# Kernel optimization log

Measured on AMD Instinct MI355X. Metric: run time of the kernel, lower is better.

Reference implementation:

```python
import jax, jax.numpy as jnp
import numpy as np

# MANO prior contact vertex indices (f1+f2+f3+f4+f5+f0 from CMap_loss3)
_F1 = [697,698,699,700,712,713,714,715,737,738,739,740,741,743,744,745,746,748,749,750,753,754,755,756,757,758,759,760,761,762,763,764,765,766,767,768]
_F2 = [46,47,48,49,164,165,166,167,194,195,223,237,238,280,281,298,301,317,320,323,324,325,326,327,328,329,330,331,332,333,340,341,342,343,344,345,346,347,348,349,350,351,352,353,354,355]
_F3 = [356,357,358,359,375,376,386,387,396,397,402,403,413,429,433,434,435,436,437,438,439,440,441,442,443,444,452,453,454,455,456,459,460,461,462,463,464,465,466,467]
_F4 = [468,469,470,471,484,485,486,496,497,506,507,513,514,524,545,546,547,548,549,550,551,552,553,555,563,564,565,566,567,570,572,573,574,575,576,577,578]
_F5 = [580,581,582,583,600,601,602,614,615,624,625,630,631,641,663,664,665,666,667,668,670,672,680,681,682,683,684,686,687,688,689,690,691,692,693,694,695]
_F0 = [73,96,98,99,772,774,775,777]
PRIOR_IDX = np.array(_F1 + _F2 + _F3 + _F4 + _F5 + _F0, dtype=np.int32)


def _sqdist(a, b):
    # a: [B,N,3], b: [B,M,3] -> squared distances [B,N,M] via ||a||^2+||b||^2-2ab
    a2 = jnp.sum(a * a, -1)          # [B,N]
    b2 = jnp.sum(b * b, -1)          # [B,M]
    ab = jnp.einsum('bnd,bmd->bnm', a, b)
    return jnp.maximum(a2[:, :, None] + b2[:, None, :] - 2.0 * ab, 0.0)


def _knn1(src, trg):
    # nearest neighbor (K=1): squared dists + indices, like pytorch3d knn_points
    d2 = _sqdist(src, trg)           # [B,N,M]
    return jnp.min(d2, -1), jnp.argmin(d2, -1)


def _verts_normals(verts, faces):
    # area-weighted vertex normals (pytorch3d verts_normals_packed)
    v0 = verts[:, faces[:, 0]]       # [B,F,3]
    v1 = verts[:, faces[:, 1]]
    v2 = verts[:, faces[:, 2]]
    fn = jnp.cross(v1 - v0, v2 - v0)
    vn = jnp.zeros_like(verts)
    vn = vn.at[:, faces[:, 0]].add(fn).at[:, faces[:, 1]].add(fn).at[:, faces[:, 2]].add(fn)
    return vn / (jnp.linalg.norm(vn, axis=-1, keepdims=True) + 1e-12)


def setup_inputs() -> dict:
    key = jax.random.key(0)
    ks = jax.random.split(key, 8)
    B, N1, V, F, Z, P = 64, 8192, 778, 1538, 64, 61
    scale = 0.1  # keep points in a 0.1 box so contact thresholds (0.005/0.01) fire
    return {
        'obj_xyz': jax.random.uniform(ks[0], (B, N1, 3), jnp.float32) * scale,
        'recon_xyz': jax.random.uniform(ks[1], (B, V, 3), jnp.float32) * scale,
        'gt_xyz': jax.random.uniform(ks[2], (B, V, 3), jnp.float32) * scale,
        'mean': jax.random.normal(ks[3], (B, Z), jnp.float32),
        'log_var': jax.random.normal(ks[4], (B, Z), jnp.float32),
        'recon_param': jax.random.normal(ks[5], (B, P), jnp.float32),
        'x_param': jax.random.normal(ks[6], (B, P), jnp.float32),
        'faces': jax.random.randint(ks[7], (F, 3), 0, V, jnp.int32),
    }


def reference(obj_xyz, recon_xyz, gt_xyz, mean, log_var, recon_param, x_param, faces):
    B = obj_xyz.shape[0]
    fB = jnp.float32(B)

    # KNN from object points to gt / reconstructed hand (squared dists)
    d_gt, _ = _knn1(obj_xyz, gt_xyz)            # [B,N1]
    d_rec, idx_rec = _knn1(obj_xyz, recon_xyz)  # [B,N1], [B,N1]

    # param loss: MSE sum / B
    param_loss = jnp.sum((recon_param - x_param) ** 2) / fB

    # CVAE loss: chamfer (point_reduction='sum', batch_reduction='mean') + KLD
    d2 = _sqdist(recon_xyz, gt_xyz)             # [B,778,778]
    recon_loss = jnp.mean(jnp.sum(jnp.min(d2, -1), -1)) + jnp.mean(jnp.sum(jnp.min(d2, -2), -1))
    KLD = -0.5 * jnp.sum(1.0 + log_var - mean ** 2 - jnp.exp(log_var)) / fB * 10.0
    cvae_loss = recon_loss + KLD

    # CMap_loss3: obj NN distance to prior hand contact verts, masked by cmap
    cmap = d_rec < 0.01 ** 2                    # [B,N1] bool
    prior = recon_xyz[:, PRIOR_IDX, :]          # [B,222,3]
    obj_CD, _ = _knn1(obj_xyz, prior)           # [B,N1]
    n_points = jnp.sum(cmap).astype(jnp.float32)
    cmap_loss = 3000.0 * jnp.sum(jnp.where(cmap, obj_CD, 0.0)) / (fB * n_points)

    # CMap consistency: contact-map overlap ratio
    recon_cmap = jnp.sqrt(d_rec) < 0.005
    gt_cmap = jnp.sqrt(d_gt) < 0.005
    gt_cnum = jnp.sum(gt_cmap).astype(jnp.float32) + 0.0001
    consistency_loss = -5.0 * jnp.sum(recon_cmap & gt_cmap).astype(jnp.float32) / gt_cnum

    # inter-penetration: gather NN hand verts/normals, sign of dot, masked dist sum
    vn = _verts_normals(recon_xyz, faces)                               # [B,778,3]
    nn_v = jnp.take_along_axis(recon_xyz, idx_rec[..., None], axis=1)   # [B,N1,3]
    nn_n = jnp.take_along_axis(vn, idx_rec[..., None], axis=1)          # [B,N1,3]
    interior = jnp.sum((nn_v - obj_xyz) * nn_n, -1) > 0                 # [B,N1]
    penetr_loss = 100.0 * jnp.sum(jnp.where(interior, d_rec, 0.0)) / fB

    a, b, c, d, e = 1.0, 0.1, 1000.0, 10.0, 10.0
    loss = a * cvae_loss + b * param_loss + c * cmap_loss + d * consistency_loss + e * penetr_loss
    return loss
```

## Files before the change

kernel.cpp:

```cpp
#include <hip/hip_runtime.h>
#include <math.h>

#define NB     64
#define N1V    8192
#define NPTS   (NB * N1V)
#define NV     778
#define NVP    780
#define NQ     195
#define SEG1Q  51
#define NFACE  1538
#define NZ     64
#define NPAR   61
#define NPRIOR 204
#define PPT    8
#define BIAS   0.0625f

#define REC_BLOCKS 256
#define GT_BLOCKS  256
#define CH_BLOCKS  128
#define NROLE_BLOCKS (REC_BLOCKS + GT_BLOCKS + CH_BLOCKS)
#define CMB_BLOCKS 64

#define BATCH_F4 2352
#define ACC_OFF (NB * BATCH_F4 * 4)
#define RC_OFF  (ACC_OFF + 16)
#define GC_OFF  (RC_OFF + NPTS / 32)

__device__ __constant__ int c_prior[NPRIOR] = {
  697,698,699,700,712,713,714,715,737,738,739,740,741,743,744,745,746,748,749,750,
  753,754,755,756,757,758,759,760,761,762,763,764,765,766,767,768,
  46,47,48,49,164,165,166,167,194,195,223,237,238,280,281,298,301,317,320,323,
  324,325,326,327,328,329,330,331,332,333,340,341,342,343,344,345,346,347,348,349,
  350,351,352,353,354,355,
  356,357,358,359,375,376,386,387,396,397,402,403,413,429,433,434,435,436,437,438,
  439,440,441,442,443,444,452,453,454,455,456,459,460,461,462,463,464,465,466,467,
  468,469,470,471,484,485,486,496,497,506,507,513,514,524,545,546,547,548,549,550,
  551,552,553,555,563,564,565,566,567,570,572,573,574,575,576,577,578,
  580,581,582,583,600,601,602,614,615,624,625,630,631,641,663,664,665,666,667,668,
  670,672,680,681,682,683,684,686,687,688,689,690,691,692,693,694,695,
  73,96,98,99,772,774,775,777
};

__global__ __launch_bounds__(256) void k_prep(const float* __restrict__ recon,
                                              const float* __restrict__ gt,
                                              const int* __restrict__ faces,
                                              float4* __restrict__ ws4,
                                              float* __restrict__ acc) {
    int b = blockIdx.x, tid = threadIdx.x;
    if (b == 0 && tid < 16) acc[tid] = 0.0f;
    __shared__ float4 s_r[NV];
    __shared__ float s_vnx[NV], s_vny[NV], s_vnz[NV];
    __shared__ unsigned int s_bm[25];
    __shared__ unsigned short s_pre[26];
    __shared__ unsigned short s_perm[NV];

    if (tid < 25) s_bm[tid] = 0u;
    __syncthreads();
    if (tid < NPRIOR) {
        int v = c_prior[tid];
        atomicOr(&s_bm[v >> 5], 1u << (v & 31));
    }
    const float* rb = recon + (size_t)b * NV * 3;
    const float* gb = gt    + (size_t)b * NV * 3;
    float4* gt4   = ws4 + (size_t)b * BATCH_F4;
    float4* rec4p = gt4 + NVP;
    float4* nrm4p = rec4p + NVP;
    for (int j = tid; j < NV; j += 256) {
        float x = rb[3*j], y = rb[3*j+1], z = rb[3*j+2];
        s_r[j] = make_float4(x, y, z, x*x + y*y + z*z + BIAS);
        x = gb[3*j]; y = gb[3*j+1]; z = gb[3*j+2];
        gt4[j] = make_float4(x, y, z, x*x + y*y + z*z);
        s_vnx[j] = 0.0f; s_vny[j] = 0.0f; s_vnz[j] = 0.0f;
    }
    if (tid < 2) gt4[NV + tid] = make_float4(0.f, 0.f, 0.f, 1e30f);
    __syncthreads();
    if (tid == 0) {
        unsigned int run = 0;
        for (int w = 0; w < 25; ++w) { s_pre[w] = (unsigned short)run; run += __popc(s_bm[w]); }
        s_pre[25] = (unsigned short)run;
    }
    __syncthreads();
    for (int j = tid; j < NV; j += 256) {
        int w = j >> 5;
        unsigned int below = s_bm[w] & ((1u << (j & 31)) - 1u);
        int rank = s_pre[w] + __popc(below);
        bool member = (s_bm[w] >> (j & 31)) & 1u;
        int pos = member ? rank : (NPRIOR + (j - rank));
        s_perm[pos] = (unsigned short)j;
    }
    for (int f = tid; f < NFACE; f += 256) {
        int i0 = faces[3*f], i1 = faces[3*f+1], i2 = faces[3*f+2];
        float4 p0 = s_r[i0], p1 = s_r[i1], p2 = s_r[i2];
        float e1x = p1.x - p0.x, e1y = p1.y - p0.y, e1z = p1.z - p0.z;
        float e2x = p2.x - p0.x, e2y = p2.y - p0.y, e2z = p2.z - p0.z;
        float fx = e1y * e2z - e1z * e2y;
        float fy = e1z * e2x - e1x * e2z;
        float fz = e1x * e2y - e1y * e2x;
        atomicAdd(&s_vnx[i0], fx); atomicAdd(&s_vny[i0], fy); atomicAdd(&s_vnz[i0], fz);
        atomicAdd(&s_vnx[i1], fx); atomicAdd(&s_vny[i1], fy); atomicAdd(&s_vnz[i1], fz);
        atomicAdd(&s_vnx[i2], fx); atomicAdd(&s_vny[i2], fy); atomicAdd(&s_vnz[i2], fz);
    }
    __syncthreads();
    for (int j = tid; j < NVP; j += 256) {
        if (j < NV) {
            int src = s_perm[j];
            rec4p[j] = s_r[src];
            float x = s_vnx[src], y = s_vny[src], z = s_vnz[src];
            float inv = 1.0f / (sqrtf(x*x + y*y + z*z) + 1e-12f);
            nrm4p[j] = make_float4(x * inv, y * inv, z * inv, 0.0f);
        } else {
            rec4p[j] = make_float4(0.f, 0.f, 0.f, 1e30f);
            nrm4p[j] = make_float4(0.f, 0.f, 1.f, 0.0f);
        }
    }
}

#define LOAD_PTS(ob)                                                          \
    const float4* ob4 = (const float4*)((ob) + (size_t)tid * 24);             \
    float4 q0 = ob4[0], q1 = ob4[1], q2 = ob4[2],                             \
           q3 = ob4[3], q4 = ob4[4], q5 = ob4[5];                             \
    float px[PPT], py[PPT], pz[PPT];                                          \
    px[0]=q0.x; py[0]=q0.y; pz[0]=q0.z;  px[1]=q0.w; py[1]=q1.x; pz[1]=q1.y;  \
    px[2]=q1.z; py[2]=q1.w; pz[2]=q2.x;  px[3]=q2.y; py[3]=q2.z; pz[3]=q2.w;  \
    px[4]=q3.x; py[4]=q3.y; pz[4]=q3.z;  px[5]=q3.w; py[5]=q4.x; pz[5]=q4.y;  \
    px[6]=q4.z; py[6]=q4.w; pz[6]=q5.x;  px[7]=q5.y; py[7]=q5.z; pz[7]=q5.w;

__global__ __launch_bounds__(256) void k_fused(const float* __restrict__ obj,
                                               const float4* __restrict__ ws4,
                                               float* __restrict__ acc,
                                               unsigned char* __restrict__ rcA,
                                               unsigned char* __restrict__ gcA) {
    __shared__ float4 s_t[NVP];
    __shared__ float s_red[3];
    int tid = threadIdx.x;
    int blk = blockIdx.x;

    if (blk < REC_BLOCKS) {
        int b = blk >> 2, chunk = blk & 3;
        const float4* base = ws4 + (size_t)b * BATCH_F4;
        const float4* rec4p = base + NVP;
        const float4* nrm4p = base + 2 * NVP;
        for (int j = tid; j < NVP; j += 256) s_t[j] = rec4p[j];
        if (tid < 3) s_red[tid] = 0.0f;
        __syncthreads();

        const float* ob = obj + ((size_t)b * N1V + (size_t)chunk * 2048) * 3;
        LOAD_PTS(ob)
        float nax[PPT], nay[PPT], naz[PPT], m[PPT];
        int q[PPT];
#pragma unroll
        for (int i = 0; i < PPT; ++i) {
            nax[i] = -2.0f * px[i]; nay[i] = -2.0f * py[i]; naz[i] = -2.0f * pz[i];
            m[i] = 3.4e38f; q[i] = 0;
        }
        float mp[PPT];
#pragma unroll 1
        for (int jq = 0; jq < SEG1Q; ++jq) {
            int j = 4 * jq;
            float4 t0 = s_t[j], t1 = s_t[j+1], t2 = s_t[j+2], t3 = s_t[j+3];
#pragma unroll
            for (int i = 0; i < PPT; ++i) {
                float d0 = fmaf(nax[i], t0.x, fmaf(nay[i], t0.y, fmaf(naz[i], t0.z, t0.w)));
                float d1 = fmaf(nax[i], t1.x, fmaf(nay[i], t1.y, fmaf(naz[i], t1.z, t1.w)));
                float d2 = fmaf(nax[i], t2.x, fmaf(nay[i], t2.y, fmaf(naz[i], t2.z, t2.w)));
                float d3 = fmaf(nax[i], t3.x, fmaf(nay[i], t3.y, fmaf(naz[i], t3.z, t3.w)));
                float mn = fminf(fminf(fminf(d0, d1), fminf(d2, d3)), m[i]);
                q[i] = (mn < m[i]) ? jq : q[i];
                m[i] = mn;
            }
        }
#pragma unroll
        for (int i = 0; i < PPT; ++i) mp[i] = m[i];
#pragma unroll 1
        for (int jq = SEG1Q; jq < NQ; ++jq) {
            int j = 4 * jq;
            float4 t0 = s_t[j], t1 = s_t[j+1], t2 = s_t[j+2], t3 = s_t[j+3];
#pragma unroll
            for (int i = 0; i < PPT; ++i) {
                float d0 = fmaf(nax[i], t0.x, fmaf(nay[i], t0.y, fmaf(naz[i], t0.z, t0.w)));
                float d1 = fmaf(nax[i], t1.x, fmaf(nay[i], t1.y, fmaf(naz[i], t1.z, t1.w)));
                float d2 = fmaf(nax[i], t2.x, fmaf(nay[i], t2.y, fmaf(naz[i], t2.z, t2.w)));
                float d3 = fmaf(nax[i], t3.x, fmaf(nay[i], t3.y, fmaf(naz[i], t3.z, t3.w)));
                float mn = fminf(fminf(fminf(d0, d1), fminf(d2, d3)), m[i]);
                q[i] = (mn < m[i]) ? jq : q[i];
                m[i] = mn;
            }
        }
        float lS_cmap = 0.0f, lN_cmap = 0.0f, lS_pen = 0.0f;
        unsigned int rcbits = 0;
#pragma unroll
        for (int i = 0; i < PPT; ++i) {
            float a2 = px[i]*px[i] + py[i]*py[i] + pz[i]*pz[i];
            float drec = fmaxf(a2 + (m[i]  - BIAS), 0.0f);
            float dpri = fmaxf(a2 + (mp[i] - BIAS), 0.0f);
            bool cm = drec < 1e-4f;
            bool rc = sqrtf(drec) < 0.005f;
            if (cm) { lS_cmap += dpri; lN_cmap += 1.0f; }
            if (rc) rcbits |= (1u << i);
            int jr = 4 * q[i];
            float4 t0 = s_t[jr], t1 = s_t[jr+1], t2 = s_t[jr+2], t3 = s_t[jr+3];
            float d0 = fmaf(nax[i], t0.x, fmaf(nay[i], t0.y, fmaf(naz[i], t0.z, t0.w)));
            float d1 = fmaf(nax[i], t1.x, fmaf(nay[i], t1.y, fmaf(naz[i], t1.z, t1.w)));
            float d2 = fmaf(nax[i], t2.x, fmaf(nay[i], t2.y, fmaf(naz[i], t2.z, t2.w)));
            float d3 = fmaf(nax[i], t3.x, fmaf(nay[i], t3.y, fmaf(naz[i], t3.z, t3.w)));
            float mmin = fminf(fminf(d0, d1), fminf(d2, d3));
            int off = (d0 == mmin) ? 0 : ((d1 == mmin) ? 1 : ((d2 == mmin) ? 2 : 3));
            int jstar = jr + off;
            float4 tS = s_t[jstar];
            float4 nr = nrm4p[jstar];
            float ddot = (tS.x - px[i]) * nr.x + (tS.y - py[i]) * nr.y
                       + (tS.z - pz[i]) * nr.z;
            if (ddot > 0.0f) lS_pen += drec;
        }
        rcA[(size_t)blk * 256 + tid] = (unsigned char)rcbits;
        atomicAdd(&s_red[0], lS_cmap);
        atomicAdd(&s_red[1], lN_cmap);
        atomicAdd(&s_red[2], lS_pen);
        __syncthreads();
        if (tid == 0) atomicAdd(&acc[3], s_red[0]);
        if (tid == 1) atomicAdd(&acc[4], s_red[1]);
        if (tid == 2) atomicAdd(&acc[7], s_red[2]);
        return;
    }

    if (blk < REC_BLOCKS + GT_BLOCKS) {
        int r = blk - REC_BLOCKS;
        int b = r >> 2, chunk = r & 3;
        const float4* gt4v = ws4 + (size_t)b * BATCH_F4;
        for (int j = tid; j < NVP; j += 256) s_t[j] = gt4v[j];
        if (tid == 0) s_red[0] = 0.0f;
        __syncthreads();

        const float* ob = obj + ((size_t)b * N1V + (size_t)chunk * 2048) * 3;
        LOAD_PTS(ob)
        float nax[PPT], nay[PPT], naz[PPT], mgt[PPT];
#pragma unroll
        for (int i = 0; i < PPT; ++i) {
            nax[i] = -2.0f * px[i]; nay[i] = -2.0f * py[i]; naz[i] = -2.0f * pz[i];
            mgt[i] = 3.4e38f;
        }
#pragma unroll 1
        for (int jq = 0; jq < NQ; ++jq) {
            int j = 4 * jq;
            float4 t0 = s_t[j], t1 = s_t[j+1], t2 = s_t[j+2], t3 = s_t[j+3];
#pragma unroll
            for (int i = 0; i < PPT; ++i) {
                float d0 = fmaf(nax[i], t0.x, fmaf(nay[i], t0.y, fmaf(naz[i], t0.z, t0.w)));
                float d1 = fmaf(nax[i], t1.x, fmaf(nay[i], t1.y, fmaf(naz[i], t1.z, t1.w)));
                float d2 = fmaf(nax[i], t2.x, fmaf(nay[i], t2.y, fmaf(naz[i], t2.z, t2.w)));
                float d3 = fmaf(nax[i], t3.x, fmaf(nay[i], t3.y, fmaf(naz[i], t3.z, t3.w)));
                mgt[i] = fminf(fminf(mgt[i], fminf(d0, d1)), fminf(d2, d3));
            }
        }
        float lN_gt = 0.0f;
        unsigned int gcbits = 0;
#pragma unroll
        for (int i = 0; i < PPT; ++i) {
            float a2 = px[i]*px[i] + py[i]*py[i] + pz[i]*pz[i];
            float dgt = fmaxf(a2 + mgt[i], 0.0f);
            if (sqrtf(dgt) < 0.005f) { lN_gt += 1.0f; gcbits |= (1u << i); }
        }
        gcA[(size_t)r * 256 + tid] = (unsigned char)gcbits;
        atomicAdd(&s_red[0], lN_gt);
        __syncthreads();
        if (tid == 0) atomicAdd(&acc[5], s_red[0]);
        return;
    }

    {
        int c   = blk - (REC_BLOCKS + GT_BLOCKS);
        int b   = c >> 1;
        int dir = c & 1;
        const float4* base = ws4 + (size_t)b * BATCH_F4;
        const float4* srcv = dir ? base : (base + NVP);
        const float4* tgtv = dir ? (base + NVP) : base;
        for (int j = tid; j < NVP; j += 256) s_t[j] = tgtv[j];
        if (tid == 0) s_red[0] = 0.0f;
        __syncthreads();

        const int CPT = 4;
        float nax[CPT], nay[CPT], naz[CPT], a2[CPT], m[CPT];
        bool valid[CPT];
#pragma unroll
        for (int k = 0; k < CPT; ++k) {
            int p = tid + 256 * k;
            valid[k] = (p < NV);
            float4 s = srcv[valid[k] ? p : 0];
            nax[k] = -2.0f * s.x; nay[k] = -2.0f * s.y; naz[k] = -2.0f * s.z;
            a2[k] = s.w;
            m[k] = 3.4e38f;
        }
#pragma unroll 1
        for (int j = 0; j < NVP; j += 4) {
            float4 t0 = s_t[j], t1 = s_t[j+1], t2 = s_t[j+2], t3 = s_t[j+3];
#pragma unroll
            for (int k = 0; k < CPT; ++k) {
                float d0 = fmaf(nax[k], t0.x, fmaf(nay[k], t0.y, fmaf(naz[k], t0.z, t0.w)));
                float d1 = fmaf(nax[k], t1.x, fmaf(nay[k], t1.y, fmaf(naz[k], t1.z, t1.w)));
                float d2 = fmaf(nax[k], t2.x, fmaf(nay[k], t2.y, fmaf(naz[k], t2.z, t2.w)));
                float d3 = fmaf(nax[k], t3.x, fmaf(nay[k], t3.y, fmaf(naz[k], t3.z, t3.w)));
                m[k] = fminf(fminf(m[k], fminf(d0, d1)), fminf(d2, d3));
            }
        }
        float local = 0.0f;
#pragma unroll
        for (int k = 0; k < CPT; ++k)
            if (valid[k]) local += fmaxf(a2[k] + m[k] - BIAS, 0.0f);
        atomicAdd(&s_red[0], local);
        __syncthreads();
        if (tid == 0) atomicAdd(&acc[2], s_red[0]);
    }
}

__global__ __launch_bounds__(256) void k_combine(float* __restrict__ acc,
                                                 const unsigned int* __restrict__ rcW,
                                                 const unsigned int* __restrict__ gcW,
                                                 const float* __restrict__ mean,
                                                 const float* __restrict__ log_var,
                                                 const float* __restrict__ rp,
                                                 const float* __restrict__ xp,
                                                 float* __restrict__ out) {
    int blk = blockIdx.x, tid = threadIdx.x;
    __shared__ float s_red[2];
    __shared__ unsigned int s_ticket;
    if (tid < 2) s_red[tid] = 0.0f;
    __syncthreads();
    int idx = blk * 256 + tid;
    unsigned int rc = rcW[idx], gc = gcW[idx];
    float cnt = (float)__popc(rc & gc);
    atomicAdd(&s_red[0], cnt);
    __syncthreads();
    if (tid == 0) atomicAdd(&acc[6], s_red[0]);
    __threadfence();
    if (tid == 0) s_ticket = atomicAdd((unsigned int*)&acc[15], 1u);
    __syncthreads();

    if (s_ticket == CMB_BLOCKS - 1) {
        if (tid < 2) s_red[tid] = 0.0f;
        __syncthreads();
        float s_param = 0.0f, s_kld = 0.0f;
        for (int i = tid; i < NB * NPAR; i += 256) {
            float d = rp[i] - xp[i];
            s_param += d * d;
        }
        for (int i = tid; i < NB * NZ; i += 256) {
            float m = mean[i], lv = log_var[i];
            s_kld += 1.0f + lv - m * m - expf(lv);
        }
        atomicAdd(&s_red[0], s_param);
        atomicAdd(&s_red[1], s_kld);
        __syncthreads();
        if (tid == 0) {
            const float fB = 64.0f;
            float a2v = atomicAdd(&acc[2], 0.0f);
            float a3  = atomicAdd(&acc[3], 0.0f);
            float a4  = atomicAdd(&acc[4], 0.0f);
            float a5  = atomicAdd(&acc[5], 0.0f);
            float a6  = atomicAdd(&acc[6], 0.0f);
            float a7  = atomicAdd(&acc[7], 0.0f);
            float param_loss  = s_red[0] / fB;
            float KLD         = -0.5f * s_red[1] / fB * 10.0f;
            float recon_loss  = a2v / fB;
            float cmap_loss   = 3000.0f * a3 / (fB * a4);
            float consistency = -5.0f * a6 / (a5 + 0.0001f);
            float penetr      = 100.0f * a7 / fB;
            out[0] = (recon_loss + KLD) + 0.1f * param_loss + 1000.0f * cmap_loss
                   + 10.0f * consistency + 10.0f * penetr;
        }
    }
}

extern "C" void kernel_launch(void* const* d_in, const int* in_sizes, int n_in,
                              void* d_out, int out_size, void* d_ws, size_t ws_size,
                              hipStream_t stream) {
    (void)in_sizes; (void)n_in; (void)out_size; (void)ws_size;
    const float* obj     = (const float*)d_in[0];
    const float* recon   = (const float*)d_in[1];
    const float* gt      = (const float*)d_in[2];
    const float* mean    = (const float*)d_in[3];
    const float* log_var = (const float*)d_in[4];
    const float* rp      = (const float*)d_in[5];
    const float* xp      = (const float*)d_in[6];
    const int*   faces   = (const int*)d_in[7];
    float* acc  = (float*)d_ws + ACC_OFF;
    float4* ws4 = (float4*)d_ws;
    unsigned char* rcA = (unsigned char*)((float*)d_ws + RC_OFF);
    unsigned char* gcA = (unsigned char*)((float*)d_ws + GC_OFF);
    float* out  = (float*)d_out;

    k_prep   <<<NB,           256, 0, stream>>>(recon, gt, faces, ws4, acc);
    k_fused  <<<NROLE_BLOCKS, 256, 0, stream>>>(obj, ws4, acc, rcA, gcA);
    k_combine<<<CMB_BLOCKS,   256, 0, stream>>>(acc, (const unsigned int*)rcA,
                                                (const unsigned int*)gcA,
                                                mean, log_var, rp, xp, out);
}
```

Baseline: 197.9 us.

## Halve block size, double block count, precompute prior permutation, use min3

The fused kernel now launches 128-thread blocks and twice as many of them, so each block covers 1024 object points (or half the hand vertices in the chamfer role). This spreads the work over more CUs on MI355X. The prior-vertex permutation is now built at compile time as a constexpr table in constant memory, replacing the bitmap, popcount and rank pass in k_prep. Min reductions are rewritten as three-input min chains so they can map to v_min3, and the inner loops are unrolled by 2. The cost is that each block reloads the 780-entry target table into shared memory twice as often, and the rcA/gcA bitmap indexing now depends on TPB.

```diff
diff --git a/kernel.cpp b/kernel.cpp
--- a/kernel.cpp
+++ b/kernel.cpp
@@ -14,10 +14,11 @@
 #define NPRIOR 204
 #define PPT    8
 #define BIAS   0.0625f
-
-#define REC_BLOCKS 256
-#define GT_BLOCKS  256
-#define CH_BLOCKS  128
+#define TPB    128
+
+#define REC_BLOCKS 512
+#define GT_BLOCKS  512
+#define CH_BLOCKS  256
 #define NROLE_BLOCKS (REC_BLOCKS + GT_BLOCKS + CH_BLOCKS)
 #define CMB_BLOCKS 64
 
@@ -26,7 +27,7 @@
 #define RC_OFF  (ACC_OFF + 16)
 #define GC_OFF  (RC_OFF + NPTS / 32)
 
-__device__ __constant__ int c_prior[NPRIOR] = {
+static constexpr int PRIOR_LIST[NPRIOR] = {
   697,698,699,700,712,713,714,715,737,738,739,740,741,743,744,745,746,748,749,750,
   753,754,755,756,757,758,759,760,761,762,763,764,765,766,767,768,
   46,47,48,49,164,165,166,167,194,195,223,237,238,280,281,298,301,317,320,323,
@@ -41,6 +42,20 @@
   73,96,98,99,772,774,775,777
 };
 
+struct PermT { unsigned short v[NV]; };
+static constexpr PermT make_perm() {
+    PermT t{};
+    bool mem[NV] = {};
+    for (int i = 0; i < NPRIOR; ++i) mem[PRIOR_LIST[i]] = true;
+    int a = 0, b = NPRIOR;
+    for (int j = 0; j < NV; ++j) {
+        if (mem[j]) t.v[a++] = (unsigned short)j;
+        else        t.v[b++] = (unsigned short)j;
+    }
+    return t;
+}
+__device__ __constant__ PermT c_perm = make_perm();
+
 __global__ __launch_bounds__(256) void k_prep(const float* __restrict__ recon,
                                               const float* __restrict__ gt,
                                               const int* __restrict__ faces,
@@ -50,16 +65,7 @@
     if (b == 0 && tid < 16) acc[tid] = 0.0f;
     __shared__ float4 s_r[NV];
     __shared__ float s_vnx[NV], s_vny[NV], s_vnz[NV];
-    __shared__ unsigned int s_bm[25];
-    __shared__ unsigned short s_pre[26];
-    __shared__ unsigned short s_perm[NV];
-
-    if (tid < 25) s_bm[tid] = 0u;
-    __syncthreads();
-    if (tid < NPRIOR) {
-        int v = c_prior[tid];
-        atomicOr(&s_bm[v >> 5], 1u << (v & 31));
-    }
+
     const float* rb = recon + (size_t)b * NV * 3;
     const float* gb = gt    + (size_t)b * NV * 3;
     float4* gt4   = ws4 + (size_t)b * BATCH_F4;
@@ -74,20 +80,6 @@
     }
     if (tid < 2) gt4[NV + tid] = make_float4(0.f, 0.f, 0.f, 1e30f);
     __syncthreads();
-    if (tid == 0) {
-        unsigned int run = 0;
-        for (int w = 0; w < 25; ++w) { s_pre[w] = (unsigned short)run; run += __popc(s_bm[w]); }
-        s_pre[25] = (unsigned short)run;
-    }
-    __syncthreads();
-    for (int j = tid; j < NV; j += 256) {
-        int w = j >> 5;
-        unsigned int below = s_bm[w] & ((1u << (j & 31)) - 1u);
-        int rank = s_pre[w] + __popc(below);
-        bool member = (s_bm[w] >> (j & 31)) & 1u;
-        int pos = member ? rank : (NPRIOR + (j - rank));
-        s_perm[pos] = (unsigned short)j;
-    }
     for (int f = tid; f < NFACE; f += 256) {
         int i0 = faces[3*f], i1 = faces[3*f+1], i2 = faces[3*f+2];
         float4 p0 = s_r[i0], p1 = s_r[i1], p2 = s_r[i2];
@@ -103,7 +95,7 @@
     __syncthreads();
     for (int j = tid; j < NVP; j += 256) {
         if (j < NV) {
-            int src = s_perm[j];
+            int src = c_perm.v[j];
             rec4p[j] = s_r[src];
             float x = s_vnx[src], y = s_vny[src], z = s_vnz[src];
             float inv = 1.0f / (sqrtf(x*x + y*y + z*z) + 1e-12f);
@@ -125,7 +117,11 @@
     px[4]=q3.x; py[4]=q3.y; pz[4]=q3.z;  px[5]=q3.w; py[5]=q4.x; pz[5]=q4.y;  \
     px[6]=q4.z; py[6]=q4.w; pz[6]=q5.x;  px[7]=q5.y; py[7]=q5.z; pz[7]=q5.w;
 
-__global__ __launch_bounds__(256) void k_fused(const float* __restrict__ obj,
+__device__ __forceinline__ float min3f(float a, float b, float c) {
+    return fminf(fminf(a, b), c);
+}
+
+__global__ __launch_bounds__(TPB) void k_fused(const float* __restrict__ obj,
                                                const float4* __restrict__ ws4,
                                                float* __restrict__ acc,
                                                unsigned char* __restrict__ rcA,
@@ -136,15 +132,15 @@
     int blk = blockIdx.x;
 
     if (blk < REC_BLOCKS) {
-        int b = blk >> 2, chunk = blk & 3;
+        int b = blk >> 3, chunk = blk & 7;
         const float4* base = ws4 + (size_t)b * BATCH_F4;
         const float4* rec4p = base + NVP;
         const float4* nrm4p = base + 2 * NVP;
-        for (int j = tid; j < NVP; j += 256) s_t[j] = rec4p[j];
+        for (int j = tid; j < NVP; j += TPB) s_t[j] = rec4p[j];
         if (tid < 3) s_red[tid] = 0.0f;
         __syncthreads();
 
-        const float* ob = obj + ((size_t)b * N1V + (size_t)chunk * 2048) * 3;
+        const float* ob = obj + ((size_t)b * N1V + (size_t)chunk * 1024) * 3;
         LOAD_PTS(ob)
         float nax[PPT], nay[PPT], naz[PPT], m[PPT];
         int q[PPT];
@@ -154,7 +150,7 @@
             m[i] = 3.4e38f; q[i] = 0;
         }
         float mp[PPT];
-#pragma unroll 1
+#pragma unroll 2
         for (int jq = 0; jq < SEG1Q; ++jq) {
             int j = 4 * jq;
             float4 t0 = s_t[j], t1 = s_t[j+1], t2 = s_t[j+2], t3 = s_t[j+3];
@@ -164,14 +160,15 @@
                 float d1 = fmaf(nax[i], t1.x, fmaf(nay[i], t1.y, fmaf(naz[i], t1.z, t1.w)));
                 float d2 = fmaf(nax[i], t2.x, fmaf(nay[i], t2.y, fmaf(naz[i], t2.z, t2.w)));
                 float d3 = fmaf(nax[i], t3.x, fmaf(nay[i], t3.y, fmaf(naz[i], t3.z, t3.w)));
-                float mn = fminf(fminf(fminf(d0, d1), fminf(d2, d3)), m[i]);
+                float u  = min3f(d0, d1, d2);
+                float mn = min3f(u, d3, m[i]);
                 q[i] = (mn < m[i]) ? jq : q[i];
                 m[i] = mn;
             }
         }
 #pragma unroll
         for (int i = 0; i < PPT; ++i) mp[i] = m[i];
-#pragma unroll 1
+#pragma unroll 2
         for (int jq = SEG1Q; jq < NQ; ++jq) {
             int j = 4 * jq;
             float4 t0 = s_t[j], t1 = s_t[j+1], t2 = s_t[j+2], t3 = s_t[j+3];
@@ -181,7 +178,8 @@
                 float d1 = fmaf(nax[i], t1.x, fmaf(nay[i], t1.y, fmaf(naz[i], t1.z, t1.w)));
                 float d2 = fmaf(nax[i], t2.x, fmaf(nay[i], t2.y, fmaf(naz[i], t2.z, t2.w)));
                 float d3 = fmaf(nax[i], t3.x, fmaf(nay[i], t3.y, fmaf(naz[i], t3.z, t3.w)));
-                float mn = fminf(fminf(fminf(d0, d1), fminf(d2, d3)), m[i]);
+                float u  = min3f(d0, d1, d2);
+                float mn = min3f(u, d3, m[i]);
                 q[i] = (mn < m[i]) ? jq : q[i];
                 m[i] = mn;
             }
@@ -212,7 +210,7 @@
                        + (tS.z - pz[i]) * nr.z;
             if (ddot > 0.0f) lS_pen += drec;
         }
-        rcA[(size_t)blk * 256 + tid] = (unsigned char)rcbits;
+        rcA[(size_t)blk * TPB + tid] = (unsigned char)rcbits;
         atomicAdd(&s_red[0], lS_cmap);
         atomicAdd(&s_red[1], lN_cmap);
         atomicAdd(&s_red[2], lS_pen);
@@ -225,13 +223,13 @@
 
     if (blk < REC_BLOCKS + GT_BLOCKS) {
         int r = blk - REC_BLOCKS;
-        int b = r >> 2, chunk = r & 3;
+        int b = r >> 3, chunk = r & 7;
         const float4* gt4v = ws4 + (size_t)b * BATCH_F4;
-        for (int j = tid; j < NVP; j += 256) s_t[j] = gt4v[j];
+        for (int j = tid; j < NVP; j += TPB) s_t[j] = gt4v[j];
         if (tid == 0) s_red[0] = 0.0f;
         __syncthreads();
 
-        const float* ob = obj + ((size_t)b * N1V + (size_t)chunk * 2048) * 3;
+        const float* ob = obj + ((size_t)b * N1V + (size_t)chunk * 1024) * 3;
         LOAD_PTS(ob)
         float nax[PPT], nay[PPT], naz[PPT], mgt[PPT];
 #pragma unroll
@@ -239,7 +237,7 @@
             nax[i] = -2.0f * px[i]; nay[i] = -2.0f * py[i]; naz[i] = -2.0f * pz[i];
             mgt[i] = 3.4e38f;
         }
-#pragma unroll 1
+#pragma unroll 2
         for (int jq = 0; jq < NQ; ++jq) {
             int j = 4 * jq;
             float4 t0 = s_t[j], t1 = s_t[j+1], t2 = s_t[j+2], t3 = s_t[j+3];
@@ -249,7 +247,8 @@
                 float d1 = fmaf(nax[i], t1.x, fmaf(nay[i], t1.y, fmaf(naz[i], t1.z, t1.w)));
                 float d2 = fmaf(nax[i], t2.x, fmaf(nay[i], t2.y, fmaf(naz[i], t2.z, t2.w)));
                 float d3 = fmaf(nax[i], t3.x, fmaf(nay[i], t3.y, fmaf(naz[i], t3.z, t3.w)));
-                mgt[i] = fminf(fminf(mgt[i], fminf(d0, d1)), fminf(d2, d3));
+                float u = min3f(d0, d1, d2);
+                mgt[i] = min3f(u, d3, mgt[i]);
             }
         }
         float lN_gt = 0.0f;
@@ -260,7 +259,7 @@
             float dgt = fmaxf(a2 + mgt[i], 0.0f);
             if (sqrtf(dgt) < 0.005f) { lN_gt += 1.0f; gcbits |= (1u << i); }
         }
-        gcA[(size_t)r * 256 + tid] = (unsigned char)gcbits;
+        gcA[(size_t)r * TPB + tid] = (unsigned char)gcbits;
         atomicAdd(&s_red[0], lN_gt);
         __syncthreads();
         if (tid == 0) atomicAdd(&acc[5], s_red[0]);
@@ -268,13 +267,15 @@
     }
 
     {
-        int c   = blk - (REC_BLOCKS + GT_BLOCKS);
-        int b   = c >> 1;
-        int dir = c & 1;
+        int c    = blk - (REC_BLOCKS + GT_BLOCKS);
+        int b    = c >> 2;
+        int sub  = c & 3;
+        int dir  = sub & 1;
+        int half = sub >> 1;
         const float4* base = ws4 + (size_t)b * BATCH_F4;
         const float4* srcv = dir ? base : (base + NVP);
         const float4* tgtv = dir ? (base + NVP) : base;
-        for (int j = tid; j < NVP; j += 256) s_t[j] = tgtv[j];
+        for (int j = tid; j < NVP; j += TPB) s_t[j] = tgtv[j];
         if (tid == 0) s_red[0] = 0.0f;
         __syncthreads();
 
@@ -283,14 +284,14 @@
         bool valid[CPT];
 #pragma unroll
         for (int k = 0; k < CPT; ++k) {
-            int p = tid + 256 * k;
+            int p = half * 512 + k * TPB + tid;
             valid[k] = (p < NV);
             float4 s = srcv[valid[k] ? p : 0];
             nax[k] = -2.0f * s.x; nay[k] = -2.0f * s.y; naz[k] = -2.0f * s.z;
             a2[k] = s.w;
             m[k] = 3.4e38f;
         }
-#pragma unroll 1
+#pragma unroll 2
         for (int j = 0; j < NVP; j += 4) {
             float4 t0 = s_t[j], t1 = s_t[j+1], t2 = s_t[j+2], t3 = s_t[j+3];
 #pragma unroll
@@ -299,7 +300,8 @@
                 float d1 = fmaf(nax[k], t1.x, fmaf(nay[k], t1.y, fmaf(naz[k], t1.z, t1.w)));
                 float d2 = fmaf(nax[k], t2.x, fmaf(nay[k], t2.y, fmaf(naz[k], t2.z, t2.w)));
                 float d3 = fmaf(nax[k], t3.x, fmaf(nay[k], t3.y, fmaf(naz[k], t3.z, t3.w)));
-                m[k] = fminf(fminf(m[k], fminf(d0, d1)), fminf(d2, d3));
+                float u = min3f(d0, d1, d2);
+                m[k] = min3f(u, d3, m[k]);
             }
         }
         float local = 0.0f;
@@ -389,7 +391,7 @@
     float* out  = (float*)d_out;
 
     k_prep   <<<NB,           256, 0, stream>>>(recon, gt, faces, ws4, acc);
-    k_fused  <<<NROLE_BLOCKS, 256, 0, stream>>>(obj, ws4, acc, rcA, gcA);
+    k_fused  <<<NROLE_BLOCKS, TPB, 0, stream>>>(obj, ws4, acc, rcA, gcA);
     k_combine<<<CMB_BLOCKS,   256, 0, stream>>>(acc, (const unsigned int*)rcA,
                                                 (const unsigned int*)gcA,
                                                 mean, log_var, rp, xp, out);
```

After: 206.9 us. 4.6% more time.
